# Kernel optimization log

Measured on AMD Instinct MI355X. Metric: run time of the kernel, lower is better.

## Reference

```python
import jax, jax.numpy as jnp
import numpy as np

B, T, C, H, W = 16, 128, 32, 16, 16
NUM_FEAT = 16
D = C * H * W            # conv1d in-channels (kernel size 1 => linear)
G = NUM_FEAT * H * W     # G3 out-channels


def setup_inputs() -> dict:
    key = jax.random.key(0)
    ks = jax.random.split(key, 8)
    s1 = 1.0 / np.sqrt(D)
    return {
        "input1": jax.random.normal(ks[0], (B, T, C, H, W), jnp.float32),
        "input2": jax.random.normal(ks[1], (B, T, C, H, W), jnp.float32),
        "w1": jax.random.uniform(ks[2], (NUM_FEAT, D), jnp.float32, -s1, s1),
        "b1": jax.random.uniform(ks[3], (NUM_FEAT,), jnp.float32, -s1, s1),
        "w2": jax.random.uniform(ks[4], (NUM_FEAT, D), jnp.float32, -s1, s1),
        "b2": jax.random.uniform(ks[5], (NUM_FEAT,), jnp.float32, -s1, s1),
        "w3": jax.random.uniform(ks[6], (G, D), jnp.float32, -s1, s1),
        "b3": jax.random.uniform(ks[7], (G,), jnp.float32, -s1, s1),
    }


def reference(input1, input2, w1, b1, w2, b2, w3, b3):
    b, t = input1.shape[:2]
    x1 = input1.reshape(b, t, D)  # [B,T,D]
    x2 = input2.reshape(b, t, D)
    # Conv1d(kernel=1) projections (channels-first conv == per-frame linear)
    q = jnp.einsum('btd,fd->btf', x1, w1) + b1          # [B,T,F]
    k = jnp.einsum('bsd,fd->bsf', x2, w2) + b2          # [B,S,F]
    scores = jnp.einsum('btf,bsf->bts', q, k)            # [B,T,T]
    attn = jax.nn.softmax(scores, axis=1)                # softmax over dim=1 (rows)
    v = jnp.einsum('bsd,gd->bsg', x1, w3) + b3           # [B,T,G]
    out = jnp.einsum('bts,bsg->btg', attn, v)            # [B,T,G]
    return out.reshape(b, t, NUM_FEAT, H, W)
```

## Files before the change

kernel.cpp:

```cpp
#include <hip/hip_runtime.h>
#include <cstdint>
#include <cstddef>

#define Bn 16
#define Tn 128
#define Dn 8192
#define Fn 16
#define Gn 4096
#define MT (Bn*Tn)

typedef __attribute__((ext_vector_type(8))) short short8;
typedef __attribute__((ext_vector_type(4))) float f32x4;

__device__ inline short f2bf(float f) {
    union { float f; uint32_t u; } c; c.f = f;
    uint32_t u = c.u;
    uint32_t r = (u + 0x7FFFu + ((u >> 16) & 1u)) >> 16;
    return (short)(r & 0xFFFFu);
}

__device__ inline short8 cvt8(float4 a, float4 b) {
    short8 v;
    v[0] = f2bf(a.x); v[1] = f2bf(a.y); v[2] = f2bf(a.z); v[3] = f2bf(a.w);
    v[4] = f2bf(b.x); v[5] = f2bf(b.y); v[6] = f2bf(b.z); v[7] = f2bf(b.w);
    return v;
}

#define N8_X1 (MT * Dn / 8)
#define N8_W3 ((size_t)Gn * Dn / 8)

__global__ __launch_bounds__(256) void cvt2_kernel(
    const float* __restrict__ x1, const float* __restrict__ w3,
    short* __restrict__ x1b, short* __restrict__ w3b)
{
    const size_t total = N8_X1 + N8_W3;
    size_t i = (size_t)blockIdx.x * 256 + threadIdx.x;
    const size_t stride = (size_t)gridDim.x * 256;
    for (; i < total; i += stride) {
        if (i < N8_X1) {
            const float4* s = ((const float4*)x1) + i * 2;
            ((short8*)x1b)[i] = cvt8(s[0], s[1]);
        } else {
            const size_t j = i - N8_X1;
            const float4* s = ((const float4*)w3) + j * 2;
            ((short8*)w3b)[j] = cvt8(s[0], s[1]);
        }
    }
}

__global__ __launch_bounds__(256) void qk_gemm_kernel(
    const short* __restrict__ x1b, const float* __restrict__ x2,
    const float* __restrict__ w1, const float* __restrict__ w2,
    const float* __restrict__ b1, const float* __restrict__ b2,
    float* __restrict__ q, float* __restrict__ k)
{
    __shared__ float red[4][16][16];
    const int tid = threadIdx.x;
    const int tile = blockIdx.x >> 1;
    const int isK  = blockIdx.x & 1;
    const int m0 = tile * 16;
    const int wave = tid >> 6, lane = tid & 63;
    const int quad = lane >> 4, r = lane & 15;
    const int kbase = wave * (Dn / 4);

    f32x4 acc = {};

    if (!isK) {
        const short* ap = x1b + (size_t)(m0 + r) * Dn + kbase + quad * 8;
        const float* bp = w1 + (size_t)r * Dn + kbase + quad * 8;
        #pragma unroll 4
        for (int it = 0; it < 64; ++it) {
            short8 af = *(const short8*)(ap + it * 32);
            const float4* b4 = (const float4*)(bp + it * 32);
            short8 bf = cvt8(b4[0], b4[1]);
            acc = __builtin_amdgcn_mfma_f32_16x16x32_bf16(af, bf, acc, 0, 0, 0);
        }
    } else {
        const float* apf = x2 + (size_t)(m0 + r) * Dn + kbase + quad * 8;
        const float* bp  = w2 + (size_t)r * Dn + kbase + quad * 8;
        #pragma unroll 4
        for (int it = 0; it < 64; ++it) {
            const float4* a4 = (const float4*)(apf + it * 32);
            short8 af = cvt8(a4[0], a4[1]);
            const float4* b4 = (const float4*)(bp + it * 32);
            short8 bf = cvt8(b4[0], b4[1]);
            acc = __builtin_amdgcn_mfma_f32_16x16x32_bf16(af, bf, acc, 0, 0, 0);
        }
    }

    #pragma unroll
    for (int reg = 0; reg < 4; ++reg)
        red[wave][quad * 4 + reg][r] = acc[reg];
    __syncthreads();

    const int m = tid >> 4, f = tid & 15;
    float s = red[0][m][f] + red[1][m][f] + red[2][m][f] + red[3][m][f];
    s += (isK ? b2 : b1)[f];
    (isK ? k : q)[(m0 + m) * Fn + f] = s;
}

__global__ __launch_bounds__(128) void attn_kernel(
    const float* __restrict__ q, const float* __restrict__ k,
    short* __restrict__ attn16)
{
    __shared__ float qs[Tn * 17];
    const int b = blockIdx.x;
    const int tid = threadIdx.x;

    for (int i = tid; i < Tn * Fn; i += 128)
        qs[(i >> 4) * 17 + (i & 15)] = q[b * Tn * Fn + i];
    __syncthreads();

    float kr[16];
    #pragma unroll
    for (int f = 0; f < 16; ++f) kr[f] = k[b * Tn * Fn + tid * Fn + f];

    float m = -1e30f, sum = 0.f;
    #pragma unroll 1
    for (int t = 0; t < Tn; ++t) {
        float sc = 0.f;
        #pragma unroll
        for (int f = 0; f < 16; ++f) sc += qs[t * 17 + f] * kr[f];
        if (sc > m) { sum = sum * __expf(m - sc) + 1.f; m = sc; }
        else        { sum += __expf(sc - m); }
    }
    const float inv = 1.f / sum;
    short* ap = attn16 + (size_t)b * Tn * Tn;
    #pragma unroll 1
    for (int t = 0; t < Tn; ++t) {
        float sc = 0.f;
        #pragma unroll
        for (int f = 0; f < 16; ++f) sc += qs[t * 17 + f] * kr[f];
        ap[t * Tn + tid] = f2bf(__expf(sc - m) * inv);
    }
}

#define BK 32

__global__ __launch_bounds__(256) void gemm_v_kernel(
    const short* __restrict__ A, const short* __restrict__ Bw,
    const float* __restrict__ bias, short* __restrict__ vT)
{
    __shared__ __attribute__((aligned(16))) short As[128 * BK];
    __shared__ __attribute__((aligned(16))) short Bs[128 * BK];

    const int tid = threadIdx.x;
    const int m0 = blockIdx.y * 128;
    const int n0 = blockIdx.x * 128;
    const int wave = tid >> 6, lane = tid & 63;
    const int wm = (wave >> 1) * 64, wn = (wave & 1) * 64;
    const int quad = lane >> 4, r = lane & 15;

    const int srow = wave * 32 + (lane >> 2);
    const int scol = (lane & 3) * 8;
    const short* gA = A  + (size_t)(m0 + srow) * Dn + scol;
    const short* gB = Bw + (size_t)(n0 + srow) * Dn + scol;
    short* lA = &As[srow * BK + scol];
    short* lB = &Bs[srow * BK + scol];

    f32x4 acc[4][4] = {};

    #pragma unroll 1
    for (int k0 = 0; k0 < Dn; k0 += BK) {
        __syncthreads();
        __builtin_amdgcn_global_load_lds(
            (const __attribute__((address_space(1))) void*)(gA + k0),
            (__attribute__((address_space(3))) void*)lA, 16, 0, 0);
        __builtin_amdgcn_global_load_lds(
            (const __attribute__((address_space(1))) void*)(gA + k0 + (size_t)16 * Dn),
            (__attribute__((address_space(3))) void*)(lA + 16 * BK), 16, 0, 0);
        __builtin_amdgcn_global_load_lds(
            (const __attribute__((address_space(1))) void*)(gB + k0),
            (__attribute__((address_space(3))) void*)lB, 16, 0, 0);
        __builtin_amdgcn_global_load_lds(
            (const __attribute__((address_space(1))) void*)(gB + k0 + (size_t)16 * Dn),
            (__attribute__((address_space(3))) void*)(lB + 16 * BK), 16, 0, 0);
        __syncthreads();

        short8 af[4], bf[4];
        #pragma unroll
        for (int i = 0; i < 4; ++i)
            af[i] = *(const short8*)&As[(wm + i * 16 + r) * BK + quad * 8];
        #pragma unroll
        for (int j = 0; j < 4; ++j)
            bf[j] = *(const short8*)&Bs[(wn + j * 16 + r) * BK + quad * 8];

        #pragma unroll
        for (int i = 0; i < 4; ++i)
            #pragma unroll
            for (int j = 0; j < 4; ++j)
                acc[i][j] = __builtin_amdgcn_mfma_f32_16x16x32_bf16(
                    af[i], bf[j], acc[i][j], 0, 0, 0);
    }

    #pragma unroll
    for (int i = 0; i < 4; ++i) {
        #pragma unroll
        for (int reg = 0; reg < 4; ++reg) {
            const int rowg = m0 + wm + i * 16 + quad * 4 + reg;
            const float bv = bias[rowg];
            #pragma unroll
            for (int j = 0; j < 4; ++j) {
                const int col = n0 + wn + j * 16 + r;
                vT[(size_t)rowg * MT + col] = f2bf(acc[i][j][reg] + bv);
            }
        }
    }
}

__global__ __launch_bounds__(256) void out_gemm_kernel(
    const short* __restrict__ attn16, const short* __restrict__ vT,
    float* __restrict__ out)
{
    __shared__ __attribute__((aligned(16))) short As[128 * BK];
    __shared__ __attribute__((aligned(16))) short Bs[128 * BK];

    const int tid = threadIdx.x;
    const int b  = blockIdx.y;
    const int n0 = blockIdx.x * 128;
    const int wave = tid >> 6, lane = tid & 63;
    const int wm = (wave >> 1) * 64, wn = (wave & 1) * 64;
    const int quad = lane >> 4, r = lane & 15;

    const int srow = wave * 32 + (lane >> 2);
    const int scol = (lane & 3) * 8;
    const short* gA = attn16 + (size_t)b * Tn * Tn + srow * Tn + scol;
    const short* gB = vT + (size_t)(n0 + srow) * MT + b * Tn + scol;
    short* lA = &As[srow * BK + scol];
    short* lB = &Bs[srow * BK + scol];

    f32x4 acc[4][4] = {};

    #pragma unroll 1
    for (int k0 = 0; k0 < Tn; k0 += BK) {
        __syncthreads();
        __builtin_amdgcn_global_load_lds(
            (const __attribute__((address_space(1))) void*)(gA + k0),
            (__attribute__((address_space(3))) void*)lA, 16, 0, 0);
        __builtin_amdgcn_global_load_lds(
            (const __attribute__((address_space(1))) void*)(gA + k0 + 16 * Tn),
            (__attribute__((address_space(3))) void*)(lA + 16 * BK), 16, 0, 0);
        __builtin_amdgcn_global_load_lds(
            (const __attribute__((address_space(1))) void*)(gB + k0),
            (__attribute__((address_space(3))) void*)lB, 16, 0, 0);
        __builtin_amdgcn_global_load_lds(
            (const __attribute__((address_space(1))) void*)(gB + k0 + (size_t)16 * MT),
            (__attribute__((address_space(3))) void*)(lB + 16 * BK), 16, 0, 0);
        __syncthreads();

        short8 af[4], bf[4];
        #pragma unroll
        for (int i = 0; i < 4; ++i)
            af[i] = *(const short8*)&As[(wm + i * 16 + r) * BK + quad * 8];
        #pragma unroll
        for (int j = 0; j < 4; ++j)
            bf[j] = *(const short8*)&Bs[(wn + j * 16 + r) * BK + quad * 8];

        #pragma unroll
        for (int i = 0; i < 4; ++i)
            #pragma unroll
            for (int j = 0; j < 4; ++j)
                acc[i][j] = __builtin_amdgcn_mfma_f32_16x16x32_bf16(
                    af[i], bf[j], acc[i][j], 0, 0, 0);
    }

    #pragma unroll
    for (int j = 0; j < 4; ++j) {
        const int col = n0 + wn + j * 16 + r;
        #pragma unroll
        for (int i = 0; i < 4; ++i) {
            #pragma unroll
            for (int reg = 0; reg < 4; ++reg) {
                const int rowt = wm + i * 16 + quad * 4 + reg;
                out[((size_t)(b * Tn + rowt)) * Gn + col] = acc[i][j][reg];
            }
        }
    }
}

extern "C" void kernel_launch(void* const* d_in, const int* in_sizes, int n_in,
                              void* d_out, int out_size, void* d_ws, size_t ws_size,
                              hipStream_t stream)
{
    const float* x1 = (const float*)d_in[0];
    const float* x2 = (const float*)d_in[1];
    const float* w1 = (const float*)d_in[2];
    const float* b1 = (const float*)d_in[3];
    const float* w2 = (const float*)d_in[4];
    const float* b2 = (const float*)d_in[5];
    const float* w3 = (const float*)d_in[6];
    const float* b3 = (const float*)d_in[7];
    float* out = (float*)d_out;

    float* q      = (float*)d_ws;
    float* k      = q + MT * Fn;
    short* attn16 = (short*)(k + MT * Fn);
    short* vT     = attn16 + (size_t)Bn * Tn * Tn;
    short* x1b    = vT + (size_t)Gn * MT;
    short* w3b    = x1b + (size_t)MT * Dn;

    cvt2_kernel<<<4096, 256, 0, stream>>>(x1, w3, x1b, w3b);
    qk_gemm_kernel<<<256, 256, 0, stream>>>(x1b, x2, w1, w2, b1, b2, q, k);
    attn_kernel<<<Bn, 128, 0, stream>>>(q, k, attn16);
    gemm_v_kernel<<<dim3(MT / 128, Gn / 128), 256, 0, stream>>>(w3b, x1b, b3, vT);
    out_gemm_kernel<<<dim3(Gn / 128, Bn), 256, 0, stream>>>(attn16, vT, out);
}
```

Before: 606.0 us.

## Split-K the V projection GEMM with fp32 partials and a reduction kernel

Splits the 8192-deep reduction of the V projection GEMM into two halves along a third grid dimension, doubling the number of workgroups. Each half writes fp32 partial results to workspace. A separate kernel then sums the partials, adds the bias and converts to bf16. This is meant to improve CU occupancy and latency hiding, but it adds roughly 128MB of extra fp32 partial-result traffic plus an extra kernel launch. The path runs only when the workspace is large enough; otherwise the original GEMM kernel is used.

```diff
diff --git a/kernel.cpp b/kernel.cpp
--- a/kernel.cpp
+++ b/kernel.cpp
@@ -136,6 +136,100 @@
 }
 
 #define BK 32
+#define KSPLIT 2
+#define KHALF (Dn / KSPLIT)
+
+__global__ __launch_bounds__(256) void gemm_v_split_kernel(
+    const short* __restrict__ A, const short* __restrict__ Bw,
+    float* __restrict__ vTf)
+{
+    __shared__ __attribute__((aligned(16))) short As[128 * BK];
+    __shared__ __attribute__((aligned(16))) short Bs[128 * BK];
+
+    const int tid = threadIdx.x;
+    const int m0 = blockIdx.y * 128;
+    const int n0 = blockIdx.x * 128;
+    const int z  = blockIdx.z;
+    const int kbase = z * KHALF;
+    float* outp = vTf + (size_t)z * Gn * MT;
+    const int wave = tid >> 6, lane = tid & 63;
+    const int wm = (wave >> 1) * 64, wn = (wave & 1) * 64;
+    const int quad = lane >> 4, r = lane & 15;
+
+    const int srow = wave * 32 + (lane >> 2);
+    const int scol = (lane & 3) * 8;
+    const short* gA = A  + (size_t)(m0 + srow) * Dn + kbase + scol;
+    const short* gB = Bw + (size_t)(n0 + srow) * Dn + kbase + scol;
+    short* lA = &As[srow * BK + scol];
+    short* lB = &Bs[srow * BK + scol];
+
+    f32x4 acc[4][4] = {};
+
+    #pragma unroll 1
+    for (int k0 = 0; k0 < KHALF; k0 += BK) {
+        __syncthreads();
+        __builtin_amdgcn_global_load_lds(
+            (const __attribute__((address_space(1))) void*)(gA + k0),
+            (__attribute__((address_space(3))) void*)lA, 16, 0, 0);
+        __builtin_amdgcn_global_load_lds(
+            (const __attribute__((address_space(1))) void*)(gA + k0 + (size_t)16 * Dn),
+            (__attribute__((address_space(3))) void*)(lA + 16 * BK), 16, 0, 0);
+        __builtin_amdgcn_global_load_lds(
+            (const __attribute__((address_space(1))) void*)(gB + k0),
+            (__attribute__((address_space(3))) void*)lB, 16, 0, 0);
+        __builtin_amdgcn_global_load_lds(
+            (const __attribute__((address_space(1))) void*)(gB + k0 + (size_t)16 * Dn),
+            (__attribute__((address_space(3))) void*)(lB + 16 * BK), 16, 0, 0);
+        __syncthreads();
+
+        short8 af[4], bf[4];
+        #pragma unroll
+        for (int i = 0; i < 4; ++i)
+            af[i] = *(const short8*)&As[(wm + i * 16 + r) * BK + quad * 8];
+        #pragma unroll
+        for (int j = 0; j < 4; ++j)
+            bf[j] = *(const short8*)&Bs[(wn + j * 16 + r) * BK + quad * 8];
+
+        #pragma unroll
+        for (int i = 0; i < 4; ++i)
+            #pragma unroll
+            for (int j = 0; j < 4; ++j)
+                acc[i][j] = __builtin_amdgcn_mfma_f32_16x16x32_bf16(
+                    af[i], bf[j], acc[i][j], 0, 0, 0);
+    }
+
+    #pragma unroll
+    for (int i = 0; i < 4; ++i) {
+        #pragma unroll
+        for (int reg = 0; reg < 4; ++reg) {
+            const int rowg = m0 + wm + i * 16 + quad * 4 + reg;
+            #pragma unroll
+            for (int j = 0; j < 4; ++j) {
+                const int col = n0 + wn + j * 16 + r;
+                outp[(size_t)rowg * MT + col] = acc[i][j][reg];
+            }
+        }
+    }
+}
+
+__global__ __launch_bounds__(256) void vt_cvt_kernel(
+    const float* __restrict__ vTf, const float* __restrict__ bias,
+    short* __restrict__ vT)
+{
+    const size_t N8 = (size_t)Gn * MT / 8;
+    const float4* p0 = (const float4*)vTf;
+    const float4* p1 = (const float4*)(vTf + (size_t)Gn * MT);
+    size_t i = (size_t)blockIdx.x * 256 + threadIdx.x;
+    const size_t stride = (size_t)gridDim.x * 256;
+    for (; i < N8; i += stride) {
+        const float bv = bias[i >> 8];
+        float4 a0 = p0[i * 2], b0 = p0[i * 2 + 1];
+        float4 a1 = p1[i * 2], b1 = p1[i * 2 + 1];
+        a0.x += a1.x + bv; a0.y += a1.y + bv; a0.z += a1.z + bv; a0.w += a1.w + bv;
+        b0.x += b1.x + bv; b0.y += b1.y + bv; b0.z += b1.z + bv; b0.w += b1.w + bv;
+        ((short8*)vT)[i] = cvt8(a0, b0);
+    }
+}
 
 __global__ __launch_bounds__(256) void gemm_v_kernel(
     const short* __restrict__ A, const short* __restrict__ Bw,
@@ -298,10 +392,27 @@
     short* vT     = attn16 + (size_t)Bn * Tn * Tn;
     short* x1b    = vT + (size_t)Gn * MT;
     short* w3b    = x1b + (size_t)MT * Dn;
+    float* vTf    = (float*)(w3b + (size_t)Gn * Dn);
+
+    const size_t need_split =
+        (size_t)MT * Fn * 4 * 2 +
+        (size_t)Bn * Tn * Tn * 2 +
+        (size_t)Gn * MT * 2 +
+        (size_t)MT * Dn * 2 +
+        (size_t)Gn * Dn * 2 +
+        (size_t)KSPLIT * Gn * MT * 4;
 
     cvt2_kernel<<<4096, 256, 0, stream>>>(x1, w3, x1b, w3b);
     qk_gemm_kernel<<<256, 256, 0, stream>>>(x1b, x2, w1, w2, b1, b2, q, k);
     attn_kernel<<<Bn, 128, 0, stream>>>(q, k, attn16);
-    gemm_v_kernel<<<dim3(MT / 128, Gn / 128), 256, 0, stream>>>(w3b, x1b, b3, vT);
+
+    if (ws_size >= need_split) {
+        gemm_v_split_kernel<<<dim3(MT / 128, Gn / 128, KSPLIT), 256, 0, stream>>>(
+            w3b, x1b, vTf);
+        vt_cvt_kernel<<<2048, 256, 0, stream>>>(vTf, b3, vT);
+    } else {
+        gemm_v_kernel<<<dim3(MT / 128, Gn / 128), 256, 0, stream>>>(w3b, x1b, b3, vT);
+    }
+
     out_gemm_kernel<<<dim3(Gn / 128, Bn), 256, 0, stream>>>(attn16, vT, out);
 }
```

Result: faster. 568.8 us (-6.1%).
